# Kernel tuning notes

Hardware: AMD Instinct MI355X
Metric: run time of the kernel (lower is better)

## Reference

```python
import jax, jax.numpy as jnp
import numpy as np

B, S, D = 4, 1024, 512
H, DK, DV = 8, 64, 64
MAX_POS = 8  # relative position clamp; w_rpr maps d_k -> max_pos+1
EPS = 1e-6
TEMP = DK ** 0.5


def setup_inputs() -> dict:
    key = jax.random.key(0)
    ks = jax.random.split(key, 10)
    inp = {
        "q": jax.random.normal(ks[0], (B, S, D), jnp.float32),
        "k": jax.random.normal(ks[1], (B, S, D), jnp.float32),
        "v": jax.random.normal(ks[2], (B, S, D), jnp.float32),
        "dist": jax.random.randint(ks[3], (B, S, S), 0, 9, jnp.int32),
        # parameters (stored [in, out]; torch Linear applies x @ W.T)
        "Wq": jax.random.normal(ks[4], (D, H * DK), jnp.float32) / np.sqrt(D),
        "Wk": jax.random.normal(ks[5], (D, H * DK), jnp.float32) / np.sqrt(D),
        "Wv": jax.random.normal(ks[6], (D, H * DV), jnp.float32) / np.sqrt(D),
        "Wrpr": jax.random.normal(ks[7], (DK, MAX_POS + 1), jnp.float32) / np.sqrt(DK),
        "Wo": jax.random.normal(ks[8], (H * DV, D), jnp.float32) / np.sqrt(H * DV),
        "ln_g": jnp.ones((D,), jnp.float32),
        "ln_b": jnp.zeros((D,), jnp.float32),
    }
    return inp


def reference(q, k, v, dist, Wq, Wk, Wv, Wrpr, Wo, ln_g, ln_b):
    residual = q
    # LayerNorm on queries only (as in the original forward)
    mu = jnp.mean(q, axis=-1, keepdims=True)
    var = jnp.var(q, axis=-1, keepdims=True)
    qn = (q - mu) / jnp.sqrt(var + EPS) * ln_g + ln_b

    # projections -> [B, H, S, d]
    qh = (qn @ Wq).reshape(B, S, H, DK).transpose(0, 2, 1, 3) / TEMP
    kh = (k @ Wk).reshape(B, S, H, DK).transpose(0, 2, 1, 3)
    vh = (v @ Wv).reshape(B, S, H, DV).transpose(0, 2, 1, 3)

    # content scores [B,H,S,S]
    attn_k = jnp.einsum("bhqd,bhkd->bhqk", qh, kh)

    # relative-position bias: project q onto rpr embeddings then gather per (query, key)
    q_dot_rpr = qh @ Wrpr  # [B,H,S,max_pos+1]
    pos = jnp.minimum(dist, MAX_POS)  # [B,S,S]
    idx = jnp.broadcast_to(pos[:, None], (B, H, S, S))
    attn_rpr = jnp.take_along_axis(q_dot_rpr, idx, axis=-1)  # [B,H,S,S]

    attn = jax.nn.softmax(attn_k + attn_rpr, axis=-1)
    out = jnp.einsum("bhqk,bhkd->bhqd", attn, vh)  # [B,H,S,DV]
    out = out.transpose(0, 2, 1, 3).reshape(B, S, H * DV)
    out = out @ Wo + residual
    return out, attn
```

## Files before the change

kernel.cpp:

```cpp
#include <hip/hip_runtime.h>

#define BB 4
#define SS 1024
#define DDIM 512
#define HH 8
#define NR 9
#define QB 16
#define EPSV 1e-6f

typedef __attribute__((ext_vector_type(8))) short bf16x8;
typedef __attribute__((ext_vector_type(4))) short short4v;
typedef __attribute__((ext_vector_type(4))) float f32x4;

struct HL { short h; short l; };

__device__ inline float bfv(short h) {
    union { unsigned u; float f; } b; b.u = ((unsigned)(unsigned short)h) << 16; return b.f;
}
__device__ inline HL split2(float x) {
    union { float f; unsigned u; } a; a.f = x;
    unsigned short hu = (unsigned short)(a.u >> 16);
    union { unsigned u; float f; } b; b.u = ((unsigned)hu) << 16;
    float r = x - b.f;
    union { float f; unsigned u; } c; c.f = r;
    HL o; o.h = (short)hu; o.l = (short)(c.u >> 16);
    return o;
}

__global__ __launch_bounds__(128) void ln_split(const float* __restrict__ q,
                                                const float* __restrict__ g,
                                                const float* __restrict__ b,
                                                short* __restrict__ yh,
                                                short* __restrict__ yl) {
    int row = blockIdx.x;
    const float* x = q + (size_t)row * DDIM;
    int t = threadIdx.x;
    float4 v = ((const float4*)x)[t];
    float s  = v.x + v.y + v.z + v.w;
    float ss = v.x*v.x + v.y*v.y + v.z*v.z + v.w*v.w;
    __shared__ float rs[128], rss[128];
    rs[t] = s; rss[t] = ss; __syncthreads();
    for (int o = 64; o > 0; o >>= 1) {
        if (t < o) { rs[t] += rs[t+o]; rss[t] += rss[t+o]; }
        __syncthreads();
    }
    float mu  = rs[0] * (1.0f/DDIM);
    float var = rss[0] * (1.0f/DDIM) - mu*mu;
    float inv = rsqrtf(var + EPSV);
    float4 gg = ((const float4*)g)[t];
    float4 bb = ((const float4*)b)[t];
    float o0 = (v.x-mu)*inv*gg.x + bb.x;
    float o1 = (v.y-mu)*inv*gg.y + bb.y;
    float o2 = (v.z-mu)*inv*gg.z + bb.z;
    float o3 = (v.w-mu)*inv*gg.w + bb.w;
    short4v h4, l4;
    HL t0 = split2(o0); h4[0] = t0.h; l4[0] = t0.l;
    HL t1 = split2(o1); h4[1] = t1.h; l4[1] = t1.l;
    HL t2 = split2(o2); h4[2] = t2.h; l4[2] = t2.l;
    HL t3 = split2(o3); h4[3] = t3.h; l4[3] = t3.l;
    *(short4v*)&yh[(size_t)row*DDIM + t*4] = h4;
    *(short4v*)&yl[(size_t)row*DDIM + t*4] = l4;
}

__global__ __launch_bounds__(256) void split_x(const float* __restrict__ x,
                                               short* __restrict__ xh,
                                               short* __restrict__ xl) {
    int i = blockIdx.x*256 + threadIdx.x;
    float4 v = ((const float4*)x)[i];
    short4v h4, l4;
    HL t0 = split2(v.x); h4[0] = t0.h; l4[0] = t0.l;
    HL t1 = split2(v.y); h4[1] = t1.h; l4[1] = t1.l;
    HL t2 = split2(v.z); h4[2] = t2.h; l4[2] = t2.l;
    HL t3 = split2(v.w); h4[3] = t3.h; l4[3] = t3.l;
    *(short4v*)&xh[(size_t)i*4] = h4;
    *(short4v*)&xl[(size_t)i*4] = l4;
}

__global__ __launch_bounds__(256) void transW(const float* __restrict__ W,
                                              short* __restrict__ wth,
                                              short* __restrict__ wtl) {
    __shared__ float T[64][65];
    int n0 = blockIdx.x*64, k0 = blockIdx.y*64;
    int t = threadIdx.x;
    int kr = t >> 4, nc = (t & 15)*4;
#pragma unroll
    for (int i = 0; i < 4; ++i) {
        float4 v = *(const float4*)&W[(size_t)(k0 + kr + i*16)*DDIM + n0 + nc];
        T[nc+0][kr+i*16] = v.x;
        T[nc+1][kr+i*16] = v.y;
        T[nc+2][kr+i*16] = v.z;
        T[nc+3][kr+i*16] = v.w;
    }
    __syncthreads();
    int nr = t >> 2, kq = (t & 3)*16;
    short h8[16], l8[16];
#pragma unroll
    for (int j = 0; j < 16; ++j) {
        HL tt = split2(T[nr][kq+j]); h8[j] = tt.h; l8[j] = tt.l;
    }
    size_t base = (size_t)(n0+nr)*DDIM + k0 + kq;
#pragma unroll
    for (int j = 0; j < 2; ++j) {
        bf16x8 hv, lv;
#pragma unroll
        for (int e = 0; e < 8; ++e) { hv[e] = h8[j*8+e]; lv[e] = l8[j*8+e]; }
        *(bf16x8*)&wth[base + j*8] = hv;
        *(bf16x8*)&wtl[base + j*8] = lv;
    }
}

template<int MODE>
__global__ __launch_bounds__(256) void mm_gemm(const short* __restrict__ Ahi,
                                               const short* __restrict__ Alo,
                                               const short* __restrict__ Bhi,
                                               const short* __restrict__ Blo,
                                               const float* __restrict__ res,
                                               short* __restrict__ o_hi,
                                               short* __restrict__ o_lo,
                                               float* __restrict__ o_f,
                                               float scale) {
    int n0 = blockIdx.x * 64, m0 = blockIdx.y * 64;
    int tid = threadIdx.x;
    int lane = tid & 63, w = tid >> 6;
    int wr = w >> 1, wc = w & 1;
    int r = lane & 15, ko = (lane >> 4) * 8;
    f32x4 acc[2][2] = {};
    int arow0 = m0 + wr*32 + r;
    int brow0 = n0 + wc*32 + r;
    for (int k0 = 0; k0 < 512; k0 += 32) {
        bf16x8 ah[2], al[2], bh[2], bl[2];
#pragma unroll
        for (int i = 0; i < 2; ++i) {
            size_t aoff = (size_t)(arow0 + i*16)*512 + k0 + ko;
            ah[i] = *(const bf16x8*)&Ahi[aoff];
            al[i] = *(const bf16x8*)&Alo[aoff];
            size_t boff = (size_t)(brow0 + i*16)*512 + k0 + ko;
            bh[i] = *(const bf16x8*)&Bhi[boff];
            bl[i] = *(const bf16x8*)&Blo[boff];
        }
#pragma unroll
        for (int i = 0; i < 2; ++i)
#pragma unroll
            for (int j = 0; j < 2; ++j) {
                acc[i][j] = __builtin_amdgcn_mfma_f32_16x16x32_bf16(ah[i], bh[j], acc[i][j], 0, 0, 0);
                acc[i][j] = __builtin_amdgcn_mfma_f32_16x16x32_bf16(ah[i], bl[j], acc[i][j], 0, 0, 0);
                acc[i][j] = __builtin_amdgcn_mfma_f32_16x16x32_bf16(al[i], bh[j], acc[i][j], 0, 0, 0);
            }
    }
    int rb = (lane >> 4) * 4;
    int cf = lane & 15;
#pragma unroll
    for (int i = 0; i < 2; ++i)
#pragma unroll
        for (int j = 0; j < 2; ++j)
#pragma unroll
            for (int rr = 0; rr < 4; ++rr) {
                int m = m0 + wr*32 + i*16 + rb + rr;
                int n = n0 + wc*32 + j*16 + cf;
                float v = acc[i][j][rr] * scale;
                if (MODE == 3) {
                    o_f[(size_t)m*512 + n] = v + res[(size_t)m*512 + n];
                } else {
                    HL tt = split2(v);
                    int b = m >> 10, s = m & 1023;
                    int hh = n >> 6, d = n & 63;
                    size_t off;
                    if (MODE == 2) off = ((size_t)((b*HH + hh)*64 + d))*SS + s;
                    else           off = ((size_t)((b*HH + hh)*SS + s))*64 + d;
                    o_hi[off] = tt.h;
                    o_lo[off] = tt.l;
                }
            }
}

__global__ __launch_bounds__(256) void qdr_kernel(const short* __restrict__ qhi,
                                                  const short* __restrict__ qlo,
                                                  const float* __restrict__ Wrpr,
                                                  float* __restrict__ qdr) {
    __shared__ float w[64*NR];
    int t = threadIdx.x;
    for (int i = t; i < 64*NR; i += 256) w[i] = Wrpr[i];
    __syncthreads();
    int row = blockIdx.x*256 + t;
    const short* qh = qhi + (size_t)row*64;
    const short* ql = qlo + (size_t)row*64;
    float acc[NR] = {};
#pragma unroll
    for (int d4 = 0; d4 < 16; ++d4) {
        short4v h4 = *(const short4v*)&qh[d4*4];
        short4v l4 = *(const short4v*)&ql[d4*4];
#pragma unroll
        for (int j = 0; j < 4; ++j) {
            float x = bfv(h4[j]) + bfv(l4[j]);
            const float* wr2 = &w[(d4*4+j)*NR];
#pragma unroll
            for (int p = 0; p < NR; ++p) acc[p] += x * wr2[p];
        }
    }
#pragma unroll
    for (int p = 0; p < NR; ++p) qdr[(size_t)row*NR + p] = acc[p];
}

__global__ __launch_bounds__(256, 2) void fused_attn(
        const short* __restrict__ qhi, const short* __restrict__ qlo,
        const short* __restrict__ khi, const short* __restrict__ klo,
        const short* __restrict__ vThi, const short* __restrict__ vTlo,
        const float* __restrict__ qdr,
        const int* __restrict__ dist,
        float* __restrict__ attn,
        short* __restrict__ pv_hi, short* __restrict__ pv_lo) {
    __shared__ float S_T[SS][QB+1];
    __shared__ float qd[QB][NR];
    __shared__ float inv_s[QB];
    int bh = blockIdx.y, b = bh >> 3, h = bh & 7;
    int q0 = blockIdx.x * QB;
    int tid = threadIdx.x, lane = tid & 63, w = tid >> 6;
    int r = lane & 15, g = lane >> 4, ko = g*8;

    if (tid < QB*NR) qd[tid/NR][tid%NR] = qdr[((size_t)bh*SS + q0)*NR + tid];

    const short* Qh = qhi + (size_t)bh*SS*64;
    const short* Ql = qlo + (size_t)bh*SS*64;
    const short* Kh = khi + (size_t)bh*SS*64;
    const short* Kl = klo + (size_t)bh*SS*64;
    f32x4 acc[16];
#pragma unroll
    for (int t2 = 0; t2 < 16; ++t2) acc[t2] = (f32x4){0.f,0.f,0.f,0.f};
#pragma unroll
    for (int ks = 0; ks < 64; ks += 32) {
        bf16x8 ah = *(const bf16x8*)&Qh[(size_t)(q0+r)*64 + ks + ko];
        bf16x8 al = *(const bf16x8*)&Ql[(size_t)(q0+r)*64 + ks + ko];
#pragma unroll
        for (int ct = 0; ct < 16; ++ct) {
            int kc = w*256 + ct*16 + r;
            bf16x8 bh2 = *(const bf16x8*)&Kh[(size_t)kc*64 + ks + ko];
            bf16x8 bl2 = *(const bf16x8*)&Kl[(size_t)kc*64 + ks + ko];
            acc[ct] = __builtin_amdgcn_mfma_f32_16x16x32_bf16(ah, bh2, acc[ct], 0, 0, 0);
            acc[ct] = __builtin_amdgcn_mfma_f32_16x16x32_bf16(ah, bl2, acc[ct], 0, 0, 0);
            acc[ct] = __builtin_amdgcn_mfma_f32_16x16x32_bf16(al, bh2, acc[ct], 0, 0, 0);
        }
    }
#pragma unroll
    for (int ct = 0; ct < 16; ++ct)
#pragma unroll
        for (int rr = 0; rr < 4; ++rr)
            S_T[w*256 + ct*16 + r][g*4 + rr] = acc[ct][rr];
    __syncthreads();

    int row = tid >> 4, c16 = tid & 15;
    const int* drow = &dist[((size_t)b*SS + q0 + row)*SS];
    float m = -1e30f;
    f32x4 sv[16];
#pragma unroll
    for (int c = 0; c < 16; ++c) {
        int col = c16*4 + c*64;
        int4 d4 = *(const int4*)&drow[col];
        f32x4 s4;
        s4[0] = S_T[col+0][row] + qd[row][d4.x > 8 ? 8 : d4.x];
        s4[1] = S_T[col+1][row] + qd[row][d4.y > 8 ? 8 : d4.y];
        s4[2] = S_T[col+2][row] + qd[row][d4.z > 8 ? 8 : d4.z];
        s4[3] = S_T[col+3][row] + qd[row][d4.w > 8 ? 8 : d4.w];
        sv[c] = s4;
        m = fmaxf(m, fmaxf(fmaxf(s4[0], s4[1]), fmaxf(s4[2], s4[3])));
    }
#pragma unroll
    for (int o = 1; o < 16; o <<= 1) m = fmaxf(m, __shfl_xor(m, o));
    float sum = 0.f;
#pragma unroll
    for (int c = 0; c < 16; ++c) {
        int col = c16*4 + c*64;
        f32x4 p4 = sv[c];
        p4[0] = expf(p4[0]-m); p4[1] = expf(p4[1]-m);
        p4[2] = expf(p4[2]-m); p4[3] = expf(p4[3]-m);
        sum += p4[0] + p4[1] + p4[2] + p4[3];
        S_T[col+0][row] = p4[0];
        S_T[col+1][row] = p4[1];
        S_T[col+2][row] = p4[2];
        S_T[col+3][row] = p4[3];
        sv[c] = p4;
    }
#pragma unroll
    for (int o = 1; o < 16; o <<= 1) sum += __shfl_xor(sum, o);
    float inv = 1.0f / sum;
    if (c16 == 0) inv_s[row] = inv;
    __syncthreads();

    float* arow = attn + ((size_t)bh*SS + q0 + row)*SS;
#pragma unroll
    for (int c = 0; c < 16; ++c) {
        int col = c16*4 + c*64;
        f32x4 o4 = sv[c];
        o4[0] *= inv; o4[1] *= inv; o4[2] *= inv; o4[3] *= inv;
        *(f32x4*)&arow[col] = o4;
    }

    const short* Vh = vThi + (size_t)bh*64*SS + (size_t)(w*16 + r)*SS;
    const short* Vl = vTlo + (size_t)bh*64*SS + (size_t)(w*16 + r)*SS;
    f32x4 oacc = (f32x4){0.f,0.f,0.f,0.f};
    for (int kb = 0; kb < SS; kb += 32) {
        int k8 = kb + ko;
        bf16x8 ah, al;
#pragma unroll
        for (int e = 0; e < 8; ++e) {
            HL tt = split2(S_T[k8 + e][r]);
            ah[e] = tt.h; al[e] = tt.l;
        }
        bf16x8 vh = *(const bf16x8*)&Vh[k8];
        bf16x8 vl = *(const bf16x8*)&Vl[k8];
        oacc = __builtin_amdgcn_mfma_f32_16x16x32_bf16(ah, vh, oacc, 0, 0, 0);
        oacc = __builtin_amdgcn_mfma_f32_16x16x32_bf16(ah, vl, oacc, 0, 0, 0);
        oacc = __builtin_amdgcn_mfma_f32_16x16x32_bf16(al, vh, oacc, 0, 0, 0);
    }
#pragma unroll
    for (int rr = 0; rr < 4; ++rr) {
        int orow = g*4 + rr;
        float val = oacc[rr] * inv_s[orow];
        HL tt = split2(val);
        size_t off = ((size_t)(b*SS + q0 + orow))*512 + h*64 + w*16 + r;
        pv_hi[off] = tt.h; pv_lo[off] = tt.l;
    }
}

extern "C" void kernel_launch(void* const* d_in, const int* in_sizes, int n_in,
                              void* d_out, int out_size, void* d_ws, size_t ws_size,
                              hipStream_t stream) {
    const float* q    = (const float*)d_in[0];
    const float* k    = (const float*)d_in[1];
    const float* v    = (const float*)d_in[2];
    const int*   dist = (const int*)d_in[3];
    const float* Wq   = (const float*)d_in[4];
    const float* Wk   = (const float*)d_in[5];
    const float* Wv   = (const float*)d_in[6];
    const float* Wrpr = (const float*)d_in[7];
    const float* Wo   = (const float*)d_in[8];
    const float* ln_g = (const float*)d_in[9];
    const float* ln_b = (const float*)d_in[10];

    float* out  = (float*)d_out;
    float* attn = out + (size_t)BB*SS*DDIM;

    const size_t NB = (size_t)BB*SS*DDIM;
    short* p = (short*)d_ws;
    short* qn_hi = p;            p += NB;
    short* qn_lo = p;            p += NB;
    short* kx_hi = p;            p += NB;
    short* kx_lo = p;            p += NB;
    short* vx_hi = p;            p += NB;
    short* vx_lo = p;            p += NB;
    short* qh_hi = p;            p += NB;
    short* qh_lo = p;            p += NB;
    short* kh_hi = p;            p += NB;
    short* kh_lo = p;            p += NB;
    short* vT_hi = p;            p += NB;
    short* vT_lo = p;            p += NB;
    short* WqT_h = p;            p += 262144;
    short* WqT_l = p;            p += 262144;
    short* WkT_h = p;            p += 262144;
    short* WkT_l = p;            p += 262144;
    short* WvT_h = p;            p += 262144;
    short* WvT_l = p;            p += 262144;
    short* WoT_h = p;            p += 262144;
    short* WoT_l = p;            p += 262144;
    float* qdrp  = (float*)p;
    short* pv_hi = qn_hi;
    short* pv_lo = qn_lo;

    ln_split<<<BB*SS, 128, 0, stream>>>(q, ln_g, ln_b, qn_hi, qn_lo);

    split_x<<<2048, 256, 0, stream>>>(k, kx_hi, kx_lo);
    split_x<<<2048, 256, 0, stream>>>(v, vx_hi, vx_lo);

    transW<<<dim3(8,8), 256, 0, stream>>>(Wq, WqT_h, WqT_l);
    transW<<<dim3(8,8), 256, 0, stream>>>(Wk, WkT_h, WkT_l);
    transW<<<dim3(8,8), 256, 0, stream>>>(Wv, WvT_h, WvT_l);
    transW<<<dim3(8,8), 256, 0, stream>>>(Wo, WoT_h, WoT_l);

    dim3 gp(8, 64);
    mm_gemm<0><<<gp, 256, 0, stream>>>(qn_hi, qn_lo, WqT_h, WqT_l, nullptr, qh_hi, qh_lo, nullptr, 0.125f);
    mm_gemm<0><<<gp, 256, 0, stream>>>(kx_hi, kx_lo, WkT_h, WkT_l, nullptr, kh_hi, kh_lo, nullptr, 1.0f);
    mm_gemm<2><<<gp, 256, 0, stream>>>(vx_hi, vx_lo, WvT_h, WvT_l, nullptr, vT_hi, vT_lo, nullptr, 1.0f);

    qdr_kernel<<<128, 256, 0, stream>>>(qh_hi, qh_lo, Wrpr, qdrp);

    fused_attn<<<dim3(SS/QB, BB*HH), 256, 0, stream>>>(qh_hi, qh_lo, kh_hi, kh_lo,
                                                       vT_hi, vT_lo, qdrp, dist,
                                                       attn, pv_hi, pv_lo);

    mm_gemm<3><<<gp, 256, 0, stream>>>(pv_hi, pv_lo, WoT_h, WoT_l, q, nullptr, nullptr, out, 1.0f);
}
```

Measured before the change: 454.6 us.

## Use 512 threads in attention with split-K PV and batch QKV GEMMs

The fused attention kernel moves from 256 to 512 threads per block. Each wave now computes half as many score columns, and the P·V product is split across two wave groups along the key dimension, with a shared-memory reduction before the output is written. The Q, K and V projection GEMMs are merged into one launch using blockIdx.z, and the output GEMM becomes its own kernel. The aim is more parallelism and fewer registers per thread in attention, plus lower launch overhead, at the cost of an extra barrier and LDS traffic for the partial sums.

```diff
diff --git a/kernel.cpp b/kernel.cpp
--- a/kernel.cpp
+++ b/kernel.cpp
@@ -109,16 +109,24 @@
     }
 }
 
-template<int MODE>
-__global__ __launch_bounds__(256) void mm_gemm(const short* __restrict__ Ahi,
-                                               const short* __restrict__ Alo,
-                                               const short* __restrict__ Bhi,
-                                               const short* __restrict__ Blo,
-                                               const float* __restrict__ res,
-                                               short* __restrict__ o_hi,
-                                               short* __restrict__ o_lo,
-                                               float* __restrict__ o_f,
-                                               float scale) {
+__global__ __launch_bounds__(256) void mm_gemm_qkv(
+        const short* __restrict__ qnh, const short* __restrict__ qnl,
+        const short* __restrict__ kxh, const short* __restrict__ kxl,
+        const short* __restrict__ vxh, const short* __restrict__ vxl,
+        const short* __restrict__ WqTh, const short* __restrict__ WqTl,
+        const short* __restrict__ WkTh, const short* __restrict__ WkTl,
+        const short* __restrict__ WvTh, const short* __restrict__ WvTl,
+        short* __restrict__ qh_hi, short* __restrict__ qh_lo,
+        short* __restrict__ kh_hi, short* __restrict__ kh_lo,
+        short* __restrict__ vT_hi, short* __restrict__ vT_lo) {
+    int z = blockIdx.z;
+    const short *Ahi, *Alo, *Bhi, *Blo;
+    short *o_hi, *o_lo;
+    float scale = 1.0f;
+    if (z == 0) { Ahi=qnh; Alo=qnl; Bhi=WqTh; Blo=WqTl; o_hi=qh_hi; o_lo=qh_lo; scale=0.125f; }
+    else if (z == 1) { Ahi=kxh; Alo=kxl; Bhi=WkTh; Blo=WkTl; o_hi=kh_hi; o_lo=kh_lo; }
+    else { Ahi=vxh; Alo=vxl; Bhi=WvTh; Blo=WvTl; o_hi=vT_hi; o_lo=vT_lo; }
+
     int n0 = blockIdx.x * 64, m0 = blockIdx.y * 64;
     int tid = threadIdx.x;
     int lane = tid & 63, w = tid >> 6;
@@ -158,18 +166,62 @@
                 int m = m0 + wr*32 + i*16 + rb + rr;
                 int n = n0 + wc*32 + j*16 + cf;
                 float v = acc[i][j][rr] * scale;
-                if (MODE == 3) {
-                    o_f[(size_t)m*512 + n] = v + res[(size_t)m*512 + n];
-                } else {
-                    HL tt = split2(v);
-                    int b = m >> 10, s = m & 1023;
-                    int hh = n >> 6, d = n & 63;
-                    size_t off;
-                    if (MODE == 2) off = ((size_t)((b*HH + hh)*64 + d))*SS + s;
-                    else           off = ((size_t)((b*HH + hh)*SS + s))*64 + d;
-                    o_hi[off] = tt.h;
-                    o_lo[off] = tt.l;
-                }
+                HL tt = split2(v);
+                int b = m >> 10, s = m & 1023;
+                int hh = n >> 6, d = n & 63;
+                size_t off;
+                if (z == 2) off = ((size_t)((b*HH + hh)*64 + d))*SS + s;
+                else        off = ((size_t)((b*HH + hh)*SS + s))*64 + d;
+                o_hi[off] = tt.h;
+                o_lo[off] = tt.l;
+            }
+}
+
+__global__ __launch_bounds__(256) void mm_gemm_o(const short* __restrict__ Ahi,
+                                                 const short* __restrict__ Alo,
+                                                 const short* __restrict__ Bhi,
+                                                 const short* __restrict__ Blo,
+                                                 const float* __restrict__ res,
+                                                 float* __restrict__ o_f) {
+    int n0 = blockIdx.x * 64, m0 = blockIdx.y * 64;
+    int tid = threadIdx.x;
+    int lane = tid & 63, w = tid >> 6;
+    int wr = w >> 1, wc = w & 1;
+    int r = lane & 15, ko = (lane >> 4) * 8;
+    f32x4 acc[2][2] = {};
+    int arow0 = m0 + wr*32 + r;
+    int brow0 = n0 + wc*32 + r;
+    for (int k0 = 0; k0 < 512; k0 += 32) {
+        bf16x8 ah[2], al[2], bh[2], bl[2];
+#pragma unroll
+        for (int i = 0; i < 2; ++i) {
+            size_t aoff = (size_t)(arow0 + i*16)*512 + k0 + ko;
+            ah[i] = *(const bf16x8*)&Ahi[aoff];
+            al[i] = *(const bf16x8*)&Alo[aoff];
+            size_t boff = (size_t)(brow0 + i*16)*512 + k0 + ko;
+            bh[i] = *(const bf16x8*)&Bhi[boff];
+            bl[i] = *(const bf16x8*)&Blo[boff];
+        }
+#pragma unroll
+        for (int i = 0; i < 2; ++i)
+#pragma unroll
+            for (int j = 0; j < 2; ++j) {
+                acc[i][j] = __builtin_amdgcn_mfma_f32_16x16x32_bf16(ah[i], bh[j], acc[i][j], 0, 0, 0);
+                acc[i][j] = __builtin_amdgcn_mfma_f32_16x16x32_bf16(ah[i], bl[j], acc[i][j], 0, 0, 0);
+                acc[i][j] = __builtin_amdgcn_mfma_f32_16x16x32_bf16(al[i], bh[j], acc[i][j], 0, 0, 0);
+            }
+    }
+    int rb = (lane >> 4) * 4;
+    int cf = lane & 15;
+#pragma unroll
+    for (int i = 0; i < 2; ++i)
+#pragma unroll
+        for (int j = 0; j < 2; ++j)
+#pragma unroll
+            for (int rr = 0; rr < 4; ++rr) {
+                int m = m0 + wr*32 + i*16 + rb + rr;
+                int n = n0 + wc*32 + j*16 + cf;
+                o_f[(size_t)m*512 + n] = acc[i][j][rr] + res[(size_t)m*512 + n];
             }
 }
 
@@ -201,7 +253,7 @@
     for (int p = 0; p < NR; ++p) qdr[(size_t)row*NR + p] = acc[p];
 }
 
-__global__ __launch_bounds__(256, 2) void fused_attn(
+__global__ __launch_bounds__(512, 4) void fused_attn(
         const short* __restrict__ qhi, const short* __restrict__ qlo,
         const short* __restrict__ khi, const short* __restrict__ klo,
         const short* __restrict__ vThi, const short* __restrict__ vTlo,
@@ -212,6 +264,7 @@
     __shared__ float S_T[SS][QB+1];
     __shared__ float qd[QB][NR];
     __shared__ float inv_s[QB];
+    __shared__ float PC[QB][68];
     int bh = blockIdx.y, b = bh >> 3, h = bh & 7;
     int q0 = blockIdx.x * QB;
     int tid = threadIdx.x, lane = tid & 63, w = tid >> 6;
@@ -223,37 +276,39 @@
     const short* Ql = qlo + (size_t)bh*SS*64;
     const short* Kh = khi + (size_t)bh*SS*64;
     const short* Kl = klo + (size_t)bh*SS*64;
-    f32x4 acc[16];
-#pragma unroll
-    for (int t2 = 0; t2 < 16; ++t2) acc[t2] = (f32x4){0.f,0.f,0.f,0.f};
-#pragma unroll
-    for (int ks = 0; ks < 64; ks += 32) {
-        bf16x8 ah = *(const bf16x8*)&Qh[(size_t)(q0+r)*64 + ks + ko];
-        bf16x8 al = *(const bf16x8*)&Ql[(size_t)(q0+r)*64 + ks + ko];
-#pragma unroll
-        for (int ct = 0; ct < 16; ++ct) {
-            int kc = w*256 + ct*16 + r;
-            bf16x8 bh2 = *(const bf16x8*)&Kh[(size_t)kc*64 + ks + ko];
-            bf16x8 bl2 = *(const bf16x8*)&Kl[(size_t)kc*64 + ks + ko];
-            acc[ct] = __builtin_amdgcn_mfma_f32_16x16x32_bf16(ah, bh2, acc[ct], 0, 0, 0);
-            acc[ct] = __builtin_amdgcn_mfma_f32_16x16x32_bf16(ah, bl2, acc[ct], 0, 0, 0);
-            acc[ct] = __builtin_amdgcn_mfma_f32_16x16x32_bf16(al, bh2, acc[ct], 0, 0, 0);
-        }
-    }
-#pragma unroll
-    for (int ct = 0; ct < 16; ++ct)
-#pragma unroll
-        for (int rr = 0; rr < 4; ++rr)
-            S_T[w*256 + ct*16 + r][g*4 + rr] = acc[ct][rr];
+    {
+        f32x4 acc[8];
+#pragma unroll
+        for (int t2 = 0; t2 < 8; ++t2) acc[t2] = (f32x4){0.f,0.f,0.f,0.f};
+#pragma unroll
+        for (int ks = 0; ks < 64; ks += 32) {
+            bf16x8 ah = *(const bf16x8*)&Qh[(size_t)(q0+r)*64 + ks + ko];
+            bf16x8 al = *(const bf16x8*)&Ql[(size_t)(q0+r)*64 + ks + ko];
+#pragma unroll
+            for (int ct = 0; ct < 8; ++ct) {
+                int kc = w*128 + ct*16 + r;
+                bf16x8 bh2 = *(const bf16x8*)&Kh[(size_t)kc*64 + ks + ko];
+                bf16x8 bl2 = *(const bf16x8*)&Kl[(size_t)kc*64 + ks + ko];
+                acc[ct] = __builtin_amdgcn_mfma_f32_16x16x32_bf16(ah, bh2, acc[ct], 0, 0, 0);
+                acc[ct] = __builtin_amdgcn_mfma_f32_16x16x32_bf16(ah, bl2, acc[ct], 0, 0, 0);
+                acc[ct] = __builtin_amdgcn_mfma_f32_16x16x32_bf16(al, bh2, acc[ct], 0, 0, 0);
+            }
+        }
+#pragma unroll
+        for (int ct = 0; ct < 8; ++ct)
+#pragma unroll
+            for (int rr = 0; rr < 4; ++rr)
+                S_T[w*128 + ct*16 + r][g*4 + rr] = acc[ct][rr];
+    }
     __syncthreads();
 
-    int row = tid >> 4, c16 = tid & 15;
+    int row = tid >> 5, c32 = tid & 31;
     const int* drow = &dist[((size_t)b*SS + q0 + row)*SS];
     float m = -1e30f;
-    f32x4 sv[16];
-#pragma unroll
-    for (int c = 0; c < 16; ++c) {
-        int col = c16*4 + c*64;
+    f32x4 sv[8];
+#pragma unroll
+    for (int c = 0; c < 8; ++c) {
+        int col = c32*4 + c*128;
         int4 d4 = *(const int4*)&drow[col];
         f32x4 s4;
         s4[0] = S_T[col+0][row] + qd[row][d4.x > 8 ? 8 : d4.x];
@@ -264,11 +319,11 @@
         m = fmaxf(m, fmaxf(fmaxf(s4[0], s4[1]), fmaxf(s4[2], s4[3])));
     }
 #pragma unroll
-    for (int o = 1; o < 16; o <<= 1) m = fmaxf(m, __shfl_xor(m, o));
+    for (int o = 1; o < 32; o <<= 1) m = fmaxf(m, __shfl_xor(m, o));
     float sum = 0.f;
 #pragma unroll
-    for (int c = 0; c < 16; ++c) {
-        int col = c16*4 + c*64;
+    for (int c = 0; c < 8; ++c) {
+        int col = c32*4 + c*128;
         f32x4 p4 = sv[c];
         p4[0] = expf(p4[0]-m); p4[1] = expf(p4[1]-m);
         p4[2] = expf(p4[2]-m); p4[3] = expf(p4[3]-m);
@@ -280,25 +335,26 @@
         sv[c] = p4;
     }
 #pragma unroll
-    for (int o = 1; o < 16; o <<= 1) sum += __shfl_xor(sum, o);
+    for (int o = 1; o < 32; o <<= 1) sum += __shfl_xor(sum, o);
     float inv = 1.0f / sum;
-    if (c16 == 0) inv_s[row] = inv;
+    if (c32 == 0) inv_s[row] = inv;
     __syncthreads();
 
     float* arow = attn + ((size_t)bh*SS + q0 + row)*SS;
 #pragma unroll
-    for (int c = 0; c < 16; ++c) {
-        int col = c16*4 + c*64;
+    for (int c = 0; c < 8; ++c) {
+        int col = c32*4 + c*128;
         f32x4 o4 = sv[c];
         o4[0] *= inv; o4[1] *= inv; o4[2] *= inv; o4[3] *= inv;
         *(f32x4*)&arow[col] = o4;
     }
 
-    const short* Vh = vThi + (size_t)bh*64*SS + (size_t)(w*16 + r)*SS;
-    const short* Vl = vTlo + (size_t)bh*64*SS + (size_t)(w*16 + r)*SS;
+    int wd = w & 3, wk = w >> 2;
+    const short* Vh = vThi + (size_t)bh*64*SS + (size_t)(wd*16 + r)*SS;
+    const short* Vl = vTlo + (size_t)bh*64*SS + (size_t)(wd*16 + r)*SS;
     f32x4 oacc = (f32x4){0.f,0.f,0.f,0.f};
-    for (int kb = 0; kb < SS; kb += 32) {
-        int k8 = kb + ko;
+    for (int kbi = 0; kbi < 16; ++kbi) {
+        int k8 = wk*512 + kbi*32 + ko;
         bf16x8 ah, al;
 #pragma unroll
         for (int e = 0; e < 8; ++e) {
@@ -311,13 +367,20 @@
         oacc = __builtin_amdgcn_mfma_f32_16x16x32_bf16(ah, vl, oacc, 0, 0, 0);
         oacc = __builtin_amdgcn_mfma_f32_16x16x32_bf16(al, vh, oacc, 0, 0, 0);
     }
-#pragma unroll
-    for (int rr = 0; rr < 4; ++rr) {
-        int orow = g*4 + rr;
-        float val = oacc[rr] * inv_s[orow];
-        HL tt = split2(val);
-        size_t off = ((size_t)(b*SS + q0 + orow))*512 + h*64 + w*16 + r;
-        pv_hi[off] = tt.h; pv_lo[off] = tt.l;
+    if (wk == 1) {
+#pragma unroll
+        for (int rr = 0; rr < 4; ++rr) PC[g*4 + rr][wd*16 + r] = oacc[rr];
+    }
+    __syncthreads();
+    if (wk == 0) {
+#pragma unroll
+        for (int rr = 0; rr < 4; ++rr) {
+            int orow = g*4 + rr;
+            float val = (oacc[rr] + PC[orow][wd*16 + r]) * inv_s[orow];
+            HL tt = split2(val);
+            size_t off = ((size_t)(b*SS + q0 + orow))*512 + h*64 + wd*16 + r;
+            pv_hi[off] = tt.h; pv_lo[off] = tt.l;
+        }
     }
 }
 
@@ -375,16 +438,16 @@
     transW<<<dim3(8,8), 256, 0, stream>>>(Wv, WvT_h, WvT_l);
     transW<<<dim3(8,8), 256, 0, stream>>>(Wo, WoT_h, WoT_l);
 
-    dim3 gp(8, 64);
-    mm_gemm<0><<<gp, 256, 0, stream>>>(qn_hi, qn_lo, WqT_h, WqT_l, nullptr, qh_hi, qh_lo, nullptr, 0.125f);
-    mm_gemm<0><<<gp, 256, 0, stream>>>(kx_hi, kx_lo, WkT_h, WkT_l, nullptr, kh_hi, kh_lo, nullptr, 1.0f);
-    mm_gemm<2><<<gp, 256, 0, stream>>>(vx_hi, vx_lo, WvT_h, WvT_l, nullptr, vT_hi, vT_lo, nullptr, 1.0f);
+    mm_gemm_qkv<<<dim3(8, 64, 3), 256, 0, stream>>>(
+        qn_hi, qn_lo, kx_hi, kx_lo, vx_hi, vx_lo,
+        WqT_h, WqT_l, WkT_h, WkT_l, WvT_h, WvT_l,
+        qh_hi, qh_lo, kh_hi, kh_lo, vT_hi, vT_lo);
 
     qdr_kernel<<<128, 256, 0, stream>>>(qh_hi, qh_lo, Wrpr, qdrp);
 
-    fused_attn<<<dim3(SS/QB, BB*HH), 256, 0, stream>>>(qh_hi, qh_lo, kh_hi, kh_lo,
+    fused_attn<<<dim3(SS/QB, BB*HH), 512, 0, stream>>>(qh_hi, qh_lo, kh_hi, kh_lo,
                                                        vT_hi, vT_lo, qdrp, dist,
                                                        attn, pv_hi, pv_lo);
 
-    mm_gemm<3><<<gp, 256, 0, stream>>>(pv_hi, pv_lo, WoT_h, WoT_l, q, nullptr, nullptr, out, 1.0f);
-}
+    mm_gemm_o<<<dim3(8, 64), 256, 0, stream>>>(pv_hi, pv_lo, WoT_h, WoT_l, q, out);
+}
```

After: 454.0 us. No clear change (-0.1%).
